# Kernel optimization log

Measured on AMD Instinct MI355X. Metric: run time of the kernel, lower is better.

Reference implementation:

```python
import jax, jax.numpy as jnp
import numpy as np

N = 100000       # nodes
E = 1_600_000    # edges (before self-loops)
NFEAT = 128
NHID = 32
HEADS = 4
HID = NHID * HEADS   # 128
NCLASS = 40
EPS = 1e-5
NEG = 0.2            # leaky_relu negative slope (GATConv default)


def setup_inputs() -> dict:
    key = jax.random.key(0)
    ks = jax.random.split(key, 32)
    s = 0.1
    d = {}
    d["x"] = jax.random.normal(ks[0], (N, NFEAT), jnp.float32)
    d["edge_index"] = jax.random.randint(ks[1], (2, E), 0, N, jnp.int32)
    # conv0: nfeat -> nhid, heads=4, concat
    d["W0"] = jax.random.normal(ks[2], (HID, NFEAT), jnp.float32) * s
    d["as0"] = jax.random.normal(ks[3], (HEADS, NHID), jnp.float32) * s
    d["ad0"] = jax.random.normal(ks[4], (HEADS, NHID), jnp.float32) * s
    d["b0"] = jnp.zeros((HID,), jnp.float32)
    d["g0"] = jnp.ones((HID,), jnp.float32)
    d["be0"] = jnp.zeros((HID,), jnp.float32)
    d["m0"] = jax.random.normal(ks[5], (HID,), jnp.float32) * 0.01
    d["v0"] = jax.random.uniform(ks[6], (HID,), jnp.float32, 0.5, 1.5)
    # conv1: hid -> nhid, heads=4, concat
    d["W1"] = jax.random.normal(ks[7], (HID, HID), jnp.float32) * s
    d["as1"] = jax.random.normal(ks[8], (HEADS, NHID), jnp.float32) * s
    d["ad1"] = jax.random.normal(ks[9], (HEADS, NHID), jnp.float32) * s
    d["b1"] = jnp.zeros((HID,), jnp.float32)
    d["g1"] = jnp.ones((HID,), jnp.float32)
    d["be1"] = jnp.zeros((HID,), jnp.float32)
    d["m1"] = jax.random.normal(ks[10], (HID,), jnp.float32) * 0.01
    d["v1"] = jax.random.uniform(ks[11], (HID,), jnp.float32, 0.5, 1.5)
    # conv_out: hid -> nclass, heads=1, concat=False
    d["W2"] = jax.random.normal(ks[12], (NCLASS, HID), jnp.float32) * s
    d["as2"] = jax.random.normal(ks[13], (1, NCLASS), jnp.float32) * s
    d["ad2"] = jax.random.normal(ks[14], (1, NCLASS), jnp.float32) * s
    d["b2"] = jnp.zeros((NCLASS,), jnp.float32)
    return d


def _gat(x, W, a_s, a_d, bias, src, dst, n, concat):
    # PyG GATConv: project, per-head attention logits, segment softmax over dst, scatter-sum
    H, C = a_s.shape
    h = (x @ W.T).reshape(n, H, C)                      # [N,H,C]
    al_s = jnp.einsum('nhc,hc->nh', h, a_s)             # [N,H]
    al_d = jnp.einsum('nhc,hc->nh', h, a_d)
    e = al_s[src] + al_d[dst]                           # [E,H]
    e = jnp.where(e > 0, e, NEG * e)                    # leaky_relu
    m = jax.ops.segment_max(e, dst, num_segments=n)     # self-loops guarantee nonempty segments
    ex = jnp.exp(e - m[dst])
    ssum = jax.ops.segment_sum(ex, dst, num_segments=n)
    alpha = ex / ssum[dst]                              # [E,H]
    out = jax.ops.segment_sum(alpha[:, :, None] * h[src], dst, num_segments=n)  # [N,H,C]
    out = out.reshape(n, H * C) if concat else out.mean(axis=1)
    return out + bias


def _bn_eval(x, g, b, m, v):
    return (x - m) * jax.lax.rsqrt(v + EPS) * g + b


def reference(x, edge_index, W0, as0, ad0, b0, g0, be0, m0, v0,
              W1, as1, ad1, b1, g1, be1, m1, v1, W2, as2, ad2, b2):
    n = x.shape[0]
    loop = jnp.arange(n, dtype=edge_index.dtype)
    src = jnp.concatenate([edge_index[0], loop])        # add_self_loops=True (PyG default)
    dst = jnp.concatenate([edge_index[1], loop])
    h = _gat(x, W0, as0, ad0, b0, src, dst, n, True)
    h = jax.nn.relu(_bn_eval(h, g0, be0, m0, v0))       # dropout is identity in eval
    h = _gat(h, W1, as1, ad1, b1, src, dst, n, True)
    h = jax.nn.relu(_bn_eval(h, g1, be1, m1, v1))
    h = _gat(h, W2, as2, ad2, b2, src, dst, n, False)
    return jax.nn.log_softmax(h, axis=1)
```

## Files before the change

kernel.cpp:

```cpp
#include <hip/hip_runtime.h>
#include <math.h>

#define NEGS 0.2f
#define EPSBN 1e-5f
#define NBIN_MAX 256
#define SBITS 9
#define SNODES 512
#define GLH 256

typedef __attribute__((ext_vector_type(8))) short short8v;
typedef __attribute__((ext_vector_type(4))) float f32x4;

static __device__ __forceinline__ float lrelu(float x){ return x > 0.f ? x : NEGS*x; }
static __device__ __forceinline__ float bf_lo(unsigned u){ return __uint_as_float(u << 16); }
static __device__ __forceinline__ float bf_hi(unsigned u){ return __uint_as_float(u & 0xffff0000u); }
static __device__ __forceinline__ float bf1(unsigned short v){ return __uint_as_float(((unsigned)v) << 16); }
static __device__ __forceinline__ unsigned short f2bf(float f){
  unsigned u = __float_as_uint(f);
  unsigned r = (u + 0x7fff + ((u >> 16) & 1)) >> 16;
  return (unsigned short)r;
}

__global__ void k_padW2(const float* __restrict__ W2, float* __restrict__ Wt2p){
  int i = blockIdx.x*256 + threadIdx.x;
  if (i >= 128*64) return;
  int k = i >> 6, c = i & 63;
  Wt2p[i] = (c < 40) ? W2[c*128 + k] : 0.f;
}

__global__ void k_scan1(const int* __restrict__ in, int* __restrict__ incl,
                        int* __restrict__ partials, int n){
  __shared__ int sd[256];
  int tid = threadIdx.x;
  int base = blockIdx.x*1024 + tid*4;
  int v[4]; int s = 0;
  #pragma unroll
  for (int j=0;j<4;++j){ int idx = base+j; v[j] = (idx<n)? in[idx] : 0; s += v[j]; }
  sd[tid] = s; __syncthreads();
  for (int off=1; off<256; off<<=1){
    int t = (tid>=off)? sd[tid-off] : 0;
    __syncthreads();
    sd[tid] += t;
    __syncthreads();
  }
  int run = sd[tid] - s;
  #pragma unroll
  for (int j=0;j<4;++j){ int idx = base+j; run += v[j]; if (idx<n) incl[idx] = run; }
  if (tid==255) partials[blockIdx.x] = sd[255];
}

__global__ void k_scan2(int* partials, int nb){
  __shared__ int sd[256];
  int tid = threadIdx.x;
  sd[tid] = (tid<nb)? partials[tid] : 0;
  __syncthreads();
  for (int off=1; off<256; off<<=1){
    int t = (tid>=off)? sd[tid-off] : 0;
    __syncthreads();
    sd[tid] += t;
    __syncthreads();
  }
  if (tid<nb) partials[tid] = sd[tid];
}

__global__ void k_scan3(int* __restrict__ offs, const int* __restrict__ partials, int n){
  int i = blockIdx.x*256 + threadIdx.x;
  if (i == 0) offs[0] = 0;
  if (i >= n) return;
  int b = i >> 10;
  if (b > 0) offs[i+1] += partials[b-1];
}

__global__ __launch_bounds__(256) void k_lhist(const int* __restrict__ ei, int E, int N,
                                               int* __restrict__ Hmat, int nbin){
  __shared__ int lh[NBIN_MAX];
  int tid = threadIdx.x;
  lh[tid] = 0;
  __syncthreads();
  int ET = E + N;
  int c0 = (int)(((long long)ET * blockIdx.x) / GLH);
  int c1 = (int)(((long long)ET * (blockIdx.x+1)) / GLH);
  for (int i = c0 + tid; i < c1; i += 256){
    int d = (i < E) ? ei[E + i] : (i - E);
    atomicAdd(&lh[d >> SBITS], 1);
  }
  __syncthreads();
  for (int b = tid; b < nbin; b += 256)
    Hmat[b*GLH + blockIdx.x] = lh[b];
}

__global__ __launch_bounds__(256) void k_write(const int* __restrict__ ei, int E, int N,
                        const int* __restrict__ Bmat, uint2* __restrict__ staged, int nbin){
  __shared__ int cur[NBIN_MAX];
  int tid = threadIdx.x;
  for (int b = tid; b < nbin; b += 256)
    cur[b] = Bmat[b*GLH + blockIdx.x];
  __syncthreads();
  int ET = E + N;
  int c0 = (int)(((long long)ET * blockIdx.x) / GLH);
  int c1 = (int)(((long long)ET * (blockIdx.x+1)) / GLH);
  for (int i = c0 + tid; i < c1; i += 256){
    int s, d;
    if (i < E){ s = ei[i]; d = ei[E+i]; } else { s = i-E; d = i-E; }
    int pos = atomicAdd(&cur[d >> SBITS], 1);
    staged[pos] = make_uint2((unsigned)s, (unsigned)d);
  }
}

__global__ __launch_bounds__(256) void k_bucket3(const uint2* __restrict__ staged,
                         const int* __restrict__ Bmat,
                         int* __restrict__ offs, int* __restrict__ csr, int N, int ET){
  __shared__ int sdeg[SNODES];
  __shared__ int sexc[SNODES];
  int b = blockIdx.x, tid = threadIdx.x;
  int node0 = b << SBITS;
  int nn = min(SNODES, N - node0);
  int base = Bmat[b*GLH];
  int cntb = Bmat[(b+1)*GLH] - base;
  sdeg[2*tid] = 0; sdeg[2*tid+1] = 0;
  __syncthreads();
  for (int e = tid; e < cntb; e += 256){
    uint2 p = staged[base + e];
    atomicAdd(&sdeg[p.y - node0], 1);
  }
  __syncthreads();
  int v0 = sdeg[2*tid], v1 = sdeg[2*tid+1];
  int ps = v0 + v1;
  sexc[tid] = ps; __syncthreads();
  for (int off=1; off<256; off<<=1){
    int t = (tid>=off)? sexc[tid-off] : 0;
    __syncthreads();
    sexc[tid] += t;
    __syncthreads();
  }
  int excl_pair = sexc[tid] - ps;
  __syncthreads();
  sexc[2*tid]   = excl_pair;
  sexc[2*tid+1] = excl_pair + v0;
  if (2*tid   < nn) offs[node0 + 2*tid]   = base + excl_pair;
  if (2*tid+1 < nn) offs[node0 + 2*tid+1] = base + excl_pair + v0;
  sdeg[2*tid] = 0; sdeg[2*tid+1] = 0;
  __syncthreads();
  for (int e = tid; e < cntb; e += 256){
    uint2 p = staged[base + e];
    int ln = p.y - node0;
    int pos = base + sexc[ln] + atomicAdd(&sdeg[ln], 1);
    csr[pos] = (int)p.x;
  }
  if (b == gridDim.x - 1 && tid == 0) offs[N] = ET;
}

template<bool BF16IN>
__global__ __launch_bounds__(256) void k_gemm128m(const void* __restrict__ Xin,
                          const float* __restrict__ W,
                          const float* __restrict__ as_, const float* __restrict__ ad_,
                          unsigned short* __restrict__ Yb,
                          float* __restrict__ ALs, float* __restrict__ ALd, int n){
  __shared__ short lds[24576];
  unsigned* ldsW = (unsigned*)lds;
  unsigned* ldsX = (unsigned*)(lds + 16384);
  int tid = threadIdx.x;
  int r0 = blockIdx.x*64;
  #pragma unroll
  for (int j=0;j<16;++j){
    int i = (256*j + tid)*4;
    int row = i >> 7;
    float4 v = *(const float4*)(W + i);
    int dw = i >> 1, lo = dw & 63, base = dw & ~63;
    int sw = base | (lo ^ ((row&7)<<2));
    uint2 p;
    p.x = (unsigned)f2bf(v.x) | ((unsigned)f2bf(v.y)<<16);
    p.y = (unsigned)f2bf(v.z) | ((unsigned)f2bf(v.w)<<16);
    *(uint2*)(&ldsW[sw]) = p;
  }
  if (!BF16IN){
    const float* X = (const float*)Xin;
    #pragma unroll
    for (int j=0;j<8;++j){
      int i = (256*j + tid)*4;
      int row = i >> 7;
      int grow = r0 + row;
      float4 v = (grow < n) ? *(const float4*)(X + (size_t)grow*128 + (i&127))
                            : make_float4(0.f,0.f,0.f,0.f);
      int dw = i >> 1, lo = dw & 63, base = dw & ~63;
      int sw = base | (lo ^ ((row&7)<<2));
      uint2 p;
      p.x = (unsigned)f2bf(v.x) | ((unsigned)f2bf(v.y)<<16);
      p.y = (unsigned)f2bf(v.z) | ((unsigned)f2bf(v.w)<<16);
      *(uint2*)(&ldsX[sw]) = p;
    }
  } else {
    const unsigned short* Xb = (const unsigned short*)Xin;
    #pragma unroll
    for (int j=0;j<4;++j){
      int dw4 = 1024*j + tid*4;
      int row = dw4 >> 6;
      int grow = r0 + row;
      uint4 v = (grow < n) ? *(const uint4*)(Xb + (size_t)grow*128 + (dw4&63)*2)
                           : make_uint4(0,0,0,0);
      int lo = dw4 & 63, base = dw4 & ~63;
      int sw = base | (lo ^ ((row&7)<<2));
      *(uint4*)(&ldsX[sw]) = v;
    }
  }
  __syncthreads();
  int l = tid & 63, w = tid >> 6;
  int lrow = l & 15, lk = l >> 4;
  int arow = w*16 + lrow;
  int abase = arow*64, ax = (arow&7)<<2;
  short8v a[4];
  #pragma unroll
  for (int ks=0;ks<4;++ks){
    int lo = ks*16 + lk*4;
    a[ks] = *(const short8v*)&ldsX[abase + (lo ^ ax)];
  }
  f32x4 acc[8];
  #pragma unroll
  for (int c=0;c<8;++c) acc[c] = (f32x4){0.f,0.f,0.f,0.f};
  #pragma unroll
  for (int c=0;c<8;++c){
    int brow = c*16 + lrow;
    int bbase2 = brow*64, bx = (brow&7)<<2;
    #pragma unroll
    for (int ks=0;ks<4;++ks){
      int lo = ks*16 + lk*4;
      short8v bfr = *(const short8v*)&ldsW[bbase2 + (lo ^ bx)];
      acc[c] = __builtin_amdgcn_mfma_f32_16x16x32_bf16(a[ks], bfr, acc[c], 0, 0, 0);
    }
  }
  __syncthreads();
  unsigned short* Ys = (unsigned short*)ldsX;
  #pragma unroll
  for (int c=0;c<8;++c){
    #pragma unroll
    for (int r=0;r<4;++r){
      int row = w*16 + lk*4 + r;
      Ys[row*128 + c*16 + lrow] = f2bf(acc[c][r]);
    }
  }
  __syncthreads();
  #pragma unroll
  for (int j=0;j<4;++j){
    int dw4 = 1024*j + tid*4;
    int row = dw4 >> 6;
    int grow = r0 + row;
    if (grow < n)
      *(uint4*)(Yb + (size_t)grow*128 + (dw4&63)*2) = *(const uint4*)&((unsigned*)ldsX)[dw4];
  }
  {
    int row = tid >> 2, h = tid & 3;
    int grow = r0 + row;
    if (grow < n){
      const unsigned short* yr = Ys + row*128 + h*32;
      float ps = 0.f, pd = 0.f;
      #pragma unroll
      for (int j=0;j<32;++j){
        float y = bf1(yr[j]);
        ps = fmaf(y, as_[h*32+j], ps);
        pd = fmaf(y, ad_[h*32+j], pd);
      }
      ALs[grow*4+h] = ps; ALd[grow*4+h] = pd;
    }
  }
}

__global__ __launch_bounds__(256) void k_agg128b(const unsigned short* __restrict__ Pb,
                         const float* __restrict__ ALs, const float* __restrict__ ALd,
                         const int* __restrict__ offs, const int* __restrict__ csr,
                         const float* __restrict__ bias, const float* __restrict__ gam,
                         const float* __restrict__ bet, const float* __restrict__ mean,
                         const float* __restrict__ var, unsigned short* __restrict__ outb, int n){
  int node = blockIdx.x*4 + (threadIdx.x >> 6);
  int lane = threadIdx.x & 63;
  if (node >= n) return;
  int el = lane >> 4, fl = lane & 15, hd = fl >> 2;
  int beg = offs[node], end = offs[node+1];
  int deg = end - beg;
  float aldw = ALd[node*4 + (lane & 3)];
  int c = (lane < deg) ? csr[beg + lane] : 0;
  float a0=0.f,a1=0.f,a2=0.f,a3=0.f,a4=0.f,a5=0.f,a6=0.f,a7=0.f;
  float wsum = 0.f;
  int nsteps = (deg + 3) >> 2;
  float wch = 0.f;
  int wbase = el*4 + hd;
  #pragma unroll 4
  for (int st = 0; st < nsteps; ++st){
    if ((st & 3) == 0){
      int we = st*4 + (lane >> 2);
      int ws = (we < 64) ? __shfl(c, we) : ((we < deg) ? csr[beg + we] : 0);
      float als = ALs[ws*4 + (lane & 3)];
      wch = (we < deg) ? __expf(lrelu(als + aldw)) : 0.f;
    }
    int idx = st*4 + el;
    float w = __shfl(wch, ((st & 3) << 4) + wbase);
    int si = (idx < 64) ? __shfl(c, idx) : ((idx < deg) ? csr[beg + idx] : 0);
    uint4 hv = *(const uint4*)(Pb + (size_t)si*128 + fl*8);
    wsum += w;
    a0 = fmaf(w, bf_lo(hv.x), a0);  a1 = fmaf(w, bf_hi(hv.x), a1);
    a2 = fmaf(w, bf_lo(hv.y), a2);  a3 = fmaf(w, bf_hi(hv.y), a3);
    a4 = fmaf(w, bf_lo(hv.z), a4);  a5 = fmaf(w, bf_hi(hv.z), a5);
    a6 = fmaf(w, bf_lo(hv.w), a6);  a7 = fmaf(w, bf_hi(hv.w), a7);
  }
  #pragma unroll
  for (int off=16; off<64; off<<=1){
    a0 += __shfl_xor(a0, off); a1 += __shfl_xor(a1, off);
    a2 += __shfl_xor(a2, off); a3 += __shfl_xor(a3, off);
    a4 += __shfl_xor(a4, off); a5 += __shfl_xor(a5, off);
    a6 += __shfl_xor(a6, off); a7 += __shfl_xor(a7, off);
    wsum += __shfl_xor(wsum, off);
  }
  if (el == 0){
    float inv = 1.f / wsum;
    int cc = fl*8;
    float4 bA = *(const float4*)(bias+cc), bB = *(const float4*)(bias+cc+4);
    float4 gA = *(const float4*)(gam+cc),  gB = *(const float4*)(gam+cc+4);
    float4 eA = *(const float4*)(bet+cc),  eB = *(const float4*)(bet+cc+4);
    float4 uA = *(const float4*)(mean+cc), uB = *(const float4*)(mean+cc+4);
    float4 vA = *(const float4*)(var+cc),  vB = *(const float4*)(var+cc+4);
    float o0 = (a0*inv + bA.x - uA.x) * rsqrtf(vA.x + EPSBN) * gA.x + eA.x;
    float o1 = (a1*inv + bA.y - uA.y) * rsqrtf(vA.y + EPSBN) * gA.y + eA.y;
    float o2 = (a2*inv + bA.z - uA.z) * rsqrtf(vA.z + EPSBN) * gA.z + eA.z;
    float o3 = (a3*inv + bA.w - uA.w) * rsqrtf(vA.w + EPSBN) * gA.w + eA.w;
    float o4 = (a4*inv + bB.x - uB.x) * rsqrtf(vB.x + EPSBN) * gB.x + eB.x;
    float o5 = (a5*inv + bB.y - uB.y) * rsqrtf(vB.y + EPSBN) * gB.y + eB.y;
    float o6 = (a6*inv + bB.z - uB.z) * rsqrtf(vB.z + EPSBN) * gB.z + eB.z;
    float o7 = (a7*inv + bB.w - uB.w) * rsqrtf(vB.w + EPSBN) * gB.w + eB.w;
    uint4 q;
    q.x = (unsigned)f2bf(fmaxf(o0,0.f)) | ((unsigned)f2bf(fmaxf(o1,0.f))<<16);
    q.y = (unsigned)f2bf(fmaxf(o2,0.f)) | ((unsigned)f2bf(fmaxf(o3,0.f))<<16);
    q.z = (unsigned)f2bf(fmaxf(o4,0.f)) | ((unsigned)f2bf(fmaxf(o5,0.f))<<16);
    q.w = (unsigned)f2bf(fmaxf(o6,0.f)) | ((unsigned)f2bf(fmaxf(o7,0.f))<<16);
    *(uint4*)(outb + (size_t)node*128 + cc) = q;
  }
}

__global__ __launch_bounds__(256) void k_gemm40n(const unsigned short* __restrict__ Gb,
                                                 const float* __restrict__ Wt2p,
                                                 const float* __restrict__ as2,
                                                 const float* __restrict__ ad2,
                                                 unsigned short* __restrict__ H2b,
                                                 float* __restrict__ al2s,
                                                 float* __restrict__ al2d, int n){
  __shared__ float xt[128*68];
  int tid = threadIdx.x;
  int r0 = blockIdx.x * 64;
  {
    int r  = tid & 63;
    int c0 = (tid >> 6) * 32;
    int row = r0 + r;
    #pragma unroll
    for (int j=0;j<4;++j){
      uint4 v = (row < n) ? *(const uint4*)(Gb + (size_t)row*128 + c0 + j*8)
                          : make_uint4(0,0,0,0);
      int k = c0 + j*8;
      xt[(k+0)*68 + r] = bf_lo(v.x);  xt[(k+1)*68 + r] = bf_hi(v.x);
      xt[(k+2)*68 + r] = bf_lo(v.y);  xt[(k+3)*68 + r] = bf_hi(v.y);
      xt[(k+4)*68 + r] = bf_lo(v.z);  xt[(k+5)*68 + r] = bf_hi(v.z);
      xt[(k+6)*68 + r] = bf_lo(v.w);  xt[(k+7)*68 + r] = bf_hi(v.w);
    }
  }
  __syncthreads();
  int tc = tid & 15, tr = tid >> 4;
  float acc[4][4] = {};
  #pragma unroll 4
  for (int k=0;k<128;++k){
    float4 wv = *(const float4*)(Wt2p + k*64 + tc*4);
    float4 xv = *(const float4*)(&xt[k*68 + tr*4]);
    float xv4[4] = {xv.x, xv.y, xv.z, xv.w};
    float wv4[4] = {wv.x, wv.y, wv.z, wv.w};
    #pragma unroll
    for (int u=0;u<4;++u)
      #pragma unroll
      for (int v=0;v<4;++v)
        acc[u][v] = fmaf(xv4[u], wv4[v], acc[u][v]);
  }
  float4 a4 = make_float4(0.f,0.f,0.f,0.f), d4 = a4;
  if (tc < 10){
    a4 = *(const float4*)(as2 + tc*4);
    d4 = *(const float4*)(ad2 + tc*4);
  }
  #pragma unroll
  for (int u=0;u<4;++u){
    int row = r0 + tr*4 + u;
    float ps = acc[u][0]*a4.x + acc[u][1]*a4.y + acc[u][2]*a4.z + acc[u][3]*a4.w;
    float pd = acc[u][0]*d4.x + acc[u][1]*d4.y + acc[u][2]*d4.z + acc[u][3]*d4.w;
    #pragma unroll
    for (int m=1; m<16; m<<=1){ ps += __shfl_xor(ps,m); pd += __shfl_xor(pd,m); }
    if (row < n){
      if (tc < 10){
        ushort4 o;
        o.x = f2bf(acc[u][0]); o.y = f2bf(acc[u][1]);
        o.z = f2bf(acc[u][2]); o.w = f2bf(acc[u][3]);
        *(ushort4*)(H2b + (size_t)row*40 + tc*4) = o;
      }
      if (tc == 0){ al2s[row] = ps; al2d[row] = pd; }
    }
  }
}

__global__ __launch_bounds__(256) void k_agg40b(const unsigned short* __restrict__ H2b,
                        const float* __restrict__ ALs, const float* __restrict__ ALd,
                        const int* __restrict__ offs, const int* __restrict__ csr,
                        const float* __restrict__ b2, float* __restrict__ out, int n){
  int node = blockIdx.x*4 + (threadIdx.x >> 6);
  int lane = threadIdx.x & 63;
  if (node >= n) return;
  int el = lane >> 3, fl = lane & 7;
  bool act = fl < 5;
  int beg = offs[node], end = offs[node+1];
  int deg = end - beg;
  float ald = ALd[node];
  int c = (lane < deg) ? csr[beg + lane] : 0;
  float a0=0.f,a1=0.f,a2=0.f,a3=0.f,a4=0.f,a5=0.f,a6=0.f,a7=0.f;
  float wsum = 0.f;
  int nsteps = (deg + 7) >> 3;
  float wch = 0.f;
  #pragma unroll 4
  for (int st = 0; st < nsteps; ++st){
    if ((st & 7) == 0){
      int we = st*8 + lane;
      int ws = (we < 64) ? __shfl(c, we) : ((we < deg) ? csr[beg + we] : 0);
      float als = ALs[ws];
      wch = (we < deg) ? __expf(lrelu(als + ald)) : 0.f;
    }
    int idx = st*8 + el;
    float w = __shfl(wch, ((st & 7) << 3) + el);
    int si = (idx < 64) ? __shfl(c, idx) : ((idx < deg) ? csr[beg + idx] : 0);
    wsum += w;
    if (act){
      uint4 hv = *(const uint4*)(H2b + (size_t)si*40 + fl*8);
      a0 = fmaf(w, bf_lo(hv.x), a0);  a1 = fmaf(w, bf_hi(hv.x), a1);
      a2 = fmaf(w, bf_lo(hv.y), a2);  a3 = fmaf(w, bf_hi(hv.y), a3);
      a4 = fmaf(w, bf_lo(hv.z), a4);  a5 = fmaf(w, bf_hi(hv.z), a5);
      a6 = fmaf(w, bf_lo(hv.w), a6);  a7 = fmaf(w, bf_hi(hv.w), a7);
    }
  }
  #pragma unroll
  for (int off=8; off<64; off<<=1){
    a0 += __shfl_xor(a0, off); a1 += __shfl_xor(a1, off);
    a2 += __shfl_xor(a2, off); a3 += __shfl_xor(a3, off);
    a4 += __shfl_xor(a4, off); a5 += __shfl_xor(a5, off);
    a6 += __shfl_xor(a6, off); a7 += __shfl_xor(a7, off);
    wsum += __shfl_xor(wsum, off);
  }
  if (el == 0){
    float inv = 1.f / wsum;
    float y0=0.f,y1=0.f,y2=0.f,y3=0.f,y4=0.f,y5=0.f,y6=0.f,y7=0.f;
    if (act){
      int cc = fl*8;
      float4 bA = *(const float4*)(b2 + cc), bB = *(const float4*)(b2 + cc + 4);
      y0 = a0*inv + bA.x; y1 = a1*inv + bA.y; y2 = a2*inv + bA.z; y3 = a3*inv + bA.w;
      y4 = a4*inv + bB.x; y5 = a5*inv + bB.y; y6 = a6*inv + bB.z; y7 = a7*inv + bB.w;
    }
    float lm = act ? fmaxf(fmaxf(fmaxf(y0,y1),fmaxf(y2,y3)),
                           fmaxf(fmaxf(y4,y5),fmaxf(y6,y7))) : -1e30f;
    lm = fmaxf(lm, __shfl_xor(lm,1));
    lm = fmaxf(lm, __shfl_xor(lm,2));
    lm = fmaxf(lm, __shfl_xor(lm,4));
    float ls = act ? (__expf(y0-lm)+__expf(y1-lm)+__expf(y2-lm)+__expf(y3-lm)
                     +__expf(y4-lm)+__expf(y5-lm)+__expf(y6-lm)+__expf(y7-lm)) : 0.f;
    ls += __shfl_xor(ls,1);
    ls += __shfl_xor(ls,2);
    ls += __shfl_xor(ls,4);
    float lg = lm + __logf(ls);
    if (act){
      float4* dst = (float4*)(out + (size_t)node*40 + fl*8);
      dst[0] = make_float4(y0-lg, y1-lg, y2-lg, y3-lg);
      dst[1] = make_float4(y4-lg, y5-lg, y6-lg, y7-lg);
    }
  }
}

extern "C" void kernel_launch(void* const* d_in, const int* in_sizes, int n_in,
                              void* d_out, int out_size, void* d_ws, size_t ws_size,
                              hipStream_t stream) {
  const float* x   = (const float*)d_in[0];
  const int*   ei  = (const int*)d_in[1];
  const float* W0  = (const float*)d_in[2];
  const float* as0 = (const float*)d_in[3];
  const float* ad0 = (const float*)d_in[4];
  const float* b0  = (const float*)d_in[5];
  const float* g0  = (const float*)d_in[6];
  const float* be0 = (const float*)d_in[7];
  const float* m0  = (const float*)d_in[8];
  const float* v0  = (const float*)d_in[9];
  const float* W1  = (const float*)d_in[10];
  const float* as1 = (const float*)d_in[11];
  const float* ad1 = (const float*)d_in[12];
  const float* b1  = (const float*)d_in[13];
  const float* g1  = (const float*)d_in[14];
  const float* be1 = (const float*)d_in[15];
  const float* m1  = (const float*)d_in[16];
  const float* v1  = (const float*)d_in[17];
  const float* W2  = (const float*)d_in[18];
  const float* as2 = (const float*)d_in[19];
  const float* ad2 = (const float*)d_in[20];
  const float* b2  = (const float*)d_in[21];
  float* out = (float*)d_out;

  int N = in_sizes[0] / 128;
  int E = in_sizes[1] / 2;
  int ET = E + N;
  int NBIN = (N + SNODES - 1) >> SBITS;
  int M = NBIN * GLH;

  char* p = (char*)d_ws;
  auto alloc = [&](size_t bytes)->void* {
    void* r = (void*)p;
    p += (bytes + 255) & ~size_t(255);
    return r;
  };
  float* Wt2p  = (float*)alloc((size_t)128*64*4);
  int* offs    = (int*)alloc((size_t)(N+1)*4);
  int* partials= (int*)alloc(1024*4);
  int* Hmat    = (int*)alloc((size_t)NBIN_MAX*GLH*4);
  int* Bmat    = (int*)alloc((size_t)(NBIN_MAX*GLH+1)*4);
  int* csr     = (int*)alloc((size_t)ET*4);
  uint2* staged= (uint2*)alloc((size_t)ET*8);
  unsigned short* Pb = (unsigned short*)alloc((size_t)N*128*2);
  unsigned short* Gb = (unsigned short*)alloc((size_t)N*128*2);
  float* ALs = (float*)alloc((size_t)N*4*4);
  float* ALd = (float*)alloc((size_t)N*4*4);
  unsigned short* H2b = Pb;
  float* al2s = ALs;
  float* al2d = ALd;
  if ((size_t)(p - (char*)d_ws) > ws_size) return;

  k_padW2<<<(128*64+255)/256, 256, 0, stream>>>(W2, Wt2p);

  k_lhist<<<GLH, 256, 0, stream>>>(ei, E, N, Hmat, NBIN);
  int nb2 = (M + 1023) / 1024;
  k_scan1<<<nb2, 256, 0, stream>>>(Hmat, Bmat+1, partials, M);
  k_scan2<<<1, 256, 0, stream>>>(partials, nb2);
  k_scan3<<<(M+255)/256, 256, 0, stream>>>(Bmat, partials, M);
  k_write<<<GLH, 256, 0, stream>>>(ei, E, N, Bmat, staged, NBIN);
  k_bucket3<<<NBIN, 256, 0, stream>>>(staged, Bmat, offs, csr, N, ET);

  int gb = (N + 63) / 64;
  k_gemm128m<false><<<gb, 256, 0, stream>>>(x, W0, as0, ad0, Pb, ALs, ALd, N);
  k_agg128b<<<(N+3)/4, 256, 0, stream>>>(Pb, ALs, ALd, offs, csr, b0, g0, be0, m0, v0, Gb, N);

  k_gemm128m<true><<<gb, 256, 0, stream>>>(Gb, W1, as1, ad1, Pb, ALs, ALd, N);
  k_agg128b<<<(N+3)/4, 256, 0, stream>>>(Pb, ALs, ALd, offs, csr, b1, g1, be1, m1, v1, Gb, N);

  k_gemm40n<<<gb, 256, 0, stream>>>(Gb, Wt2p, as2, ad2, H2b, al2s, al2d, N);
  k_agg40b<<<(N+3)/4, 256, 0, stream>>>(H2b, al2s, al2d, offs, csr, b2, out, N);
}
```

Measured before the change: 498.3 us.

## Pack staged edges, pre-convert weights to bf16, prefetch gathers in aggregation

Several independent changes. Staged edge pairs are packed into one 32-bit word (source index plus local destination), halving the staging traffic in the CSR build. W0 and W1 are converted to bf16 once in a prep kernel, so each GEMM block copies them without converting. The aggregation kernels now compute all attention weights for the first 64 edges up front, software-prefetch the next neighbor row inside the loop, and handle degrees above 64 in a separate tail loop. The tail loop and the 23-bit source packing assume source indices below about 8 million.

```diff
diff --git a/kernel.cpp b/kernel.cpp
--- a/kernel.cpp
+++ b/kernel.cpp
@@ -21,11 +21,17 @@
   return (unsigned short)r;
 }
 
-__global__ void k_padW2(const float* __restrict__ W2, float* __restrict__ Wt2p){
+__global__ void k_prep(const float* __restrict__ W0, const float* __restrict__ W1,
+                       const float* __restrict__ W2, unsigned short* __restrict__ Wb0,
+                       unsigned short* __restrict__ Wb1, float* __restrict__ Wt2p){
   int i = blockIdx.x*256 + threadIdx.x;
-  if (i >= 128*64) return;
-  int k = i >> 6, c = i & 63;
-  Wt2p[i] = (c < 40) ? W2[c*128 + k] : 0.f;
+  if (i < 16384){ Wb0[i] = f2bf(W0[i]); return; }
+  if (i < 32768){ Wb1[i-16384] = f2bf(W1[i-16384]); return; }
+  if (i < 40960){
+    int j = i - 32768;
+    int k = j >> 6, c = j & 63;
+    Wt2p[j] = (c < 40) ? W2[c*128 + k] : 0.f;
+  }
 }
 
 __global__ void k_scan1(const int* __restrict__ in, int* __restrict__ incl,
@@ -90,7 +96,7 @@
 }
 
 __global__ __launch_bounds__(256) void k_write(const int* __restrict__ ei, int E, int N,
-                        const int* __restrict__ Bmat, uint2* __restrict__ staged, int nbin){
+                        const int* __restrict__ Bmat, unsigned* __restrict__ staged, int nbin){
   __shared__ int cur[NBIN_MAX];
   int tid = threadIdx.x;
   for (int b = tid; b < nbin; b += 256)
@@ -103,11 +109,11 @@
     int s, d;
     if (i < E){ s = ei[i]; d = ei[E+i]; } else { s = i-E; d = i-E; }
     int pos = atomicAdd(&cur[d >> SBITS], 1);
-    staged[pos] = make_uint2((unsigned)s, (unsigned)d);
-  }
-}
-
-__global__ __launch_bounds__(256) void k_bucket3(const uint2* __restrict__ staged,
+    staged[pos] = (unsigned)s | ((unsigned)(d & (SNODES-1)) << 23);
+  }
+}
+
+__global__ __launch_bounds__(256) void k_bucket3(const unsigned* __restrict__ staged,
                          const int* __restrict__ Bmat,
                          int* __restrict__ offs, int* __restrict__ csr, int N, int ET){
   __shared__ int sdeg[SNODES];
@@ -120,8 +126,8 @@
   sdeg[2*tid] = 0; sdeg[2*tid+1] = 0;
   __syncthreads();
   for (int e = tid; e < cntb; e += 256){
-    uint2 p = staged[base + e];
-    atomicAdd(&sdeg[p.y - node0], 1);
+    unsigned p = staged[base + e];
+    atomicAdd(&sdeg[p >> 23], 1);
   }
   __syncthreads();
   int v0 = sdeg[2*tid], v1 = sdeg[2*tid+1];
@@ -142,17 +148,17 @@
   sdeg[2*tid] = 0; sdeg[2*tid+1] = 0;
   __syncthreads();
   for (int e = tid; e < cntb; e += 256){
-    uint2 p = staged[base + e];
-    int ln = p.y - node0;
+    unsigned p = staged[base + e];
+    int ln = p >> 23;
     int pos = base + sexc[ln] + atomicAdd(&sdeg[ln], 1);
-    csr[pos] = (int)p.x;
+    csr[pos] = (int)(p & 0x7FFFFFu);
   }
   if (b == gridDim.x - 1 && tid == 0) offs[N] = ET;
 }
 
 template<bool BF16IN>
 __global__ __launch_bounds__(256) void k_gemm128m(const void* __restrict__ Xin,
-                          const float* __restrict__ W,
+                          const unsigned short* __restrict__ Wb,
                           const float* __restrict__ as_, const float* __restrict__ ad_,
                           unsigned short* __restrict__ Yb,
                           float* __restrict__ ALs, float* __restrict__ ALd, int n){
@@ -162,16 +168,12 @@
   int tid = threadIdx.x;
   int r0 = blockIdx.x*64;
   #pragma unroll
-  for (int j=0;j<16;++j){
-    int i = (256*j + tid)*4;
-    int row = i >> 7;
-    float4 v = *(const float4*)(W + i);
-    int dw = i >> 1, lo = dw & 63, base = dw & ~63;
-    int sw = base | (lo ^ ((row&7)<<2));
-    uint2 p;
-    p.x = (unsigned)f2bf(v.x) | ((unsigned)f2bf(v.y)<<16);
-    p.y = (unsigned)f2bf(v.z) | ((unsigned)f2bf(v.w)<<16);
-    *(uint2*)(&ldsW[sw]) = p;
+  for (int j=0;j<8;++j){
+    int dw4 = 1024*j + tid*4;
+    int row = dw4 >> 6;
+    uint4 v = *(const uint4*)(Wb + (size_t)dw4*2);
+    int lo = dw4 & 63, base = dw4 & ~63;
+    *(uint4*)(&ldsW[base | (lo ^ ((row&7)<<2))]) = v;
   }
   if (!BF16IN){
     const float* X = (const float*)Xin;
@@ -278,28 +280,55 @@
   int deg = end - beg;
   float aldw = ALd[node*4 + (lane & 3)];
   int c = (lane < deg) ? csr[beg + lane] : 0;
+  float w0, w1, w2, w3;
+  {
+    int e0 = lane >> 2, h0 = lane & 3;
+    int s0 = __shfl(c, e0), s1 = __shfl(c, 16+e0);
+    int s2 = __shfl(c, 32+e0), s3 = __shfl(c, 48+e0);
+    float al0 = ALs[s0*4+h0], al1 = ALs[s1*4+h0];
+    float al2 = ALs[s2*4+h0], al3 = ALs[s3*4+h0];
+    w0 = (e0      < deg) ? __expf(lrelu(al0 + aldw)) : 0.f;
+    w1 = (16 + e0 < deg) ? __expf(lrelu(al1 + aldw)) : 0.f;
+    w2 = (32 + e0 < deg) ? __expf(lrelu(al2 + aldw)) : 0.f;
+    w3 = (48 + e0 < deg) ? __expf(lrelu(al3 + aldw)) : 0.f;
+  }
   float a0=0.f,a1=0.f,a2=0.f,a3=0.f,a4=0.f,a5=0.f,a6=0.f,a7=0.f;
   float wsum = 0.f;
   int nsteps = (deg + 3) >> 2;
-  float wch = 0.f;
-  int wbase = el*4 + hd;
-  #pragma unroll 4
-  for (int st = 0; st < nsteps; ++st){
-    if ((st & 3) == 0){
-      int we = st*4 + (lane >> 2);
-      int ws = (we < 64) ? __shfl(c, we) : ((we < deg) ? csr[beg + we] : 0);
-      float als = ALs[ws*4 + (lane & 3)];
-      wch = (we < deg) ? __expf(lrelu(als + aldw)) : 0.f;
-    }
-    int idx = st*4 + el;
-    float w = __shfl(wch, ((st & 3) << 4) + wbase);
-    int si = (idx < 64) ? __shfl(c, idx) : ((idx < deg) ? csr[beg + idx] : 0);
-    uint4 hv = *(const uint4*)(Pb + (size_t)si*128 + fl*8);
+  int ns64 = min(nsteps, 16);
+  uint4 hv;
+  {
+    int si = __shfl(c, el);
+    hv = *(const uint4*)(Pb + (size_t)si*128 + fl*8);
+  }
+  for (int st = 0; st < ns64; ++st){
+    int q = st >> 2, r = st & 3;
+    float wc = (q==0) ? w0 : (q==1) ? w1 : (q==2) ? w2 : w3;
+    float w = __shfl(wc, (r*4 + el)*4 + hd);
+    uint4 hvN = make_uint4(0,0,0,0);
+    if (st + 1 < ns64){
+      int siN = __shfl(c, (st+1)*4 + el);
+      hvN = *(const uint4*)(Pb + (size_t)siN*128 + fl*8);
+    }
     wsum += w;
     a0 = fmaf(w, bf_lo(hv.x), a0);  a1 = fmaf(w, bf_hi(hv.x), a1);
     a2 = fmaf(w, bf_lo(hv.y), a2);  a3 = fmaf(w, bf_hi(hv.y), a3);
     a4 = fmaf(w, bf_lo(hv.z), a4);  a5 = fmaf(w, bf_hi(hv.z), a5);
     a6 = fmaf(w, bf_lo(hv.w), a6);  a7 = fmaf(w, bf_hi(hv.w), a7);
+    hv = hvN;
+  }
+  if (deg > 64){
+    float aldh = __shfl(aldw, hd);
+    for (int idx = 64 + el; idx < deg; idx += 4){
+      int si = csr[beg + idx];
+      float w = __expf(lrelu(ALs[si*4 + hd] + aldh));
+      uint4 h4 = *(const uint4*)(Pb + (size_t)si*128 + fl*8);
+      wsum += w;
+      a0 = fmaf(w, bf_lo(h4.x), a0);  a1 = fmaf(w, bf_hi(h4.x), a1);
+      a2 = fmaf(w, bf_lo(h4.y), a2);  a3 = fmaf(w, bf_hi(h4.y), a3);
+      a4 = fmaf(w, bf_lo(h4.z), a4);  a5 = fmaf(w, bf_hi(h4.z), a5);
+      a6 = fmaf(w, bf_lo(h4.w), a6);  a7 = fmaf(w, bf_hi(h4.w), a7);
+    }
   }
   #pragma unroll
   for (int off=16; off<64; off<<=1){
@@ -411,28 +440,42 @@
   int deg = end - beg;
   float ald = ALd[node];
   int c = (lane < deg) ? csr[beg + lane] : 0;
+  float wch = (lane < deg) ? __expf(lrelu(ALs[c] + ald)) : 0.f;
   float a0=0.f,a1=0.f,a2=0.f,a3=0.f,a4=0.f,a5=0.f,a6=0.f,a7=0.f;
   float wsum = 0.f;
   int nsteps = (deg + 7) >> 3;
-  float wch = 0.f;
-  #pragma unroll 4
-  for (int st = 0; st < nsteps; ++st){
-    if ((st & 7) == 0){
-      int we = st*8 + lane;
-      int ws = (we < 64) ? __shfl(c, we) : ((we < deg) ? csr[beg + we] : 0);
-      float als = ALs[ws];
-      wch = (we < deg) ? __expf(lrelu(als + ald)) : 0.f;
-    }
-    int idx = st*8 + el;
-    float w = __shfl(wch, ((st & 7) << 3) + el);
-    int si = (idx < 64) ? __shfl(c, idx) : ((idx < deg) ? csr[beg + idx] : 0);
+  int ns64 = min(nsteps, 8);
+  uint4 hv = make_uint4(0,0,0,0);
+  {
+    int si = __shfl(c, el);
+    if (act) hv = *(const uint4*)(H2b + (size_t)si*40 + fl*8);
+  }
+  for (int st = 0; st < ns64; ++st){
+    float w = __shfl(wch, st*8 + el);
+    uint4 hvN = make_uint4(0,0,0,0);
+    if (st + 1 < ns64){
+      int siN = __shfl(c, (st+1)*8 + el);
+      if (act) hvN = *(const uint4*)(H2b + (size_t)siN*40 + fl*8);
+    }
     wsum += w;
-    if (act){
-      uint4 hv = *(const uint4*)(H2b + (size_t)si*40 + fl*8);
-      a0 = fmaf(w, bf_lo(hv.x), a0);  a1 = fmaf(w, bf_hi(hv.x), a1);
-      a2 = fmaf(w, bf_lo(hv.y), a2);  a3 = fmaf(w, bf_hi(hv.y), a3);
-      a4 = fmaf(w, bf_lo(hv.z), a4);  a5 = fmaf(w, bf_hi(hv.z), a5);
-      a6 = fmaf(w, bf_lo(hv.w), a6);  a7 = fmaf(w, bf_hi(hv.w), a7);
+    a0 = fmaf(w, bf_lo(hv.x), a0);  a1 = fmaf(w, bf_hi(hv.x), a1);
+    a2 = fmaf(w, bf_lo(hv.y), a2);  a3 = fmaf(w, bf_hi(hv.y), a3);
+    a4 = fmaf(w, bf_lo(hv.z), a4);  a5 = fmaf(w, bf_hi(hv.z), a5);
+    a6 = fmaf(w, bf_lo(hv.w), a6);  a7 = fmaf(w, bf_hi(hv.w), a7);
+    hv = hvN;
+  }
+  if (deg > 64){
+    for (int idx = 64 + el; idx < deg; idx += 8){
+      int si = csr[beg + idx];
+      float w = __expf(lrelu(ALs[si] + ald));
+      wsum += w;
+      if (act){
+        uint4 h4 = *(const uint4*)(H2b + (size_t)si*40 + fl*8);
+        a0 = fmaf(w, bf_lo(h4.x), a0);  a1 = fmaf(w, bf_hi(h4.x), a1);
+        a2 = fmaf(w, bf_lo(h4.y), a2);  a3 = fmaf(w, bf_hi(h4.y), a3);
+        a4 = fmaf(w, bf_lo(h4.z), a4);  a5 = fmaf(w, bf_hi(h4.z), a5);
+        a6 = fmaf(w, bf_lo(h4.w), a6);  a7 = fmaf(w, bf_hi(h4.w), a7);
+      }
     }
   }
   #pragma unroll
@@ -510,13 +553,15 @@
     p += (bytes + 255) & ~size_t(255);
     return r;
   };
+  unsigned short* Wb0 = (unsigned short*)alloc((size_t)128*128*2);
+  unsigned short* Wb1 = (unsigned short*)alloc((size_t)128*128*2);
   float* Wt2p  = (float*)alloc((size_t)128*64*4);
   int* offs    = (int*)alloc((size_t)(N+1)*4);
   int* partials= (int*)alloc(1024*4);
   int* Hmat    = (int*)alloc((size_t)NBIN_MAX*GLH*4);
   int* Bmat    = (int*)alloc((size_t)(NBIN_MAX*GLH+1)*4);
   int* csr     = (int*)alloc((size_t)ET*4);
-  uint2* staged= (uint2*)alloc((size_t)ET*8);
+  unsigned* staged = (unsigned*)alloc((size_t)ET*4);
   unsigned short* Pb = (unsigned short*)alloc((size_t)N*128*2);
   unsigned short* Gb = (unsigned short*)alloc((size_t)N*128*2);
   float* ALs = (float*)alloc((size_t)N*4*4);
@@ -526,7 +571,7 @@
   float* al2d = ALd;
   if ((size_t)(p - (char*)d_ws) > ws_size) return;
 
-  k_padW2<<<(128*64+255)/256, 256, 0, stream>>>(W2, Wt2p);
+  k_prep<<<(40960+255)/256, 256, 0, stream>>>(W0, W1, W2, Wb0, Wb1, Wt2p);
 
   k_lhist<<<GLH, 256, 0, stream>>>(ei, E, N, Hmat, NBIN);
   int nb2 = (M + 1023) / 1024;
@@ -537,10 +582,10 @@
   k_bucket3<<<NBIN, 256, 0, stream>>>(staged, Bmat, offs, csr, N, ET);
 
   int gb = (N + 63) / 64;
-  k_gemm128m<false><<<gb, 256, 0, stream>>>(x, W0, as0, ad0, Pb, ALs, ALd, N);
+  k_gemm128m<false><<<gb, 256, 0, stream>>>(x, Wb0, as0, ad0, Pb, ALs, ALd, N);
   k_agg128b<<<(N+3)/4, 256, 0, stream>>>(Pb, ALs, ALd, offs, csr, b0, g0, be0, m0, v0, Gb, N);
 
-  k_gemm128m<true><<<gb, 256, 0, stream>>>(Gb, W1, as1, ad1, Pb, ALs, ALd, N);
+  k_gemm128m<true><<<gb, 256, 0, stream>>>(Gb, Wb1, as1, ad1, Pb, ALs, ALd, N);
   k_agg128b<<<(N+3)/4, 256, 0, stream>>>(Pb, ALs, ALd, offs, csr, b1, g1, be1, m1, v1, Gb, N);
 
   k_gemm40n<<<gb, 256, 0, stream>>>(Gb, Wt2p, as2, ad2, H2b, al2s, al2d, N);
```

After: 481.6 us. 1.03x faster.
